# Kernel optimization log

Hardware: AMD Instinct MI355X
Metric: run time of the kernel (lower is better)

The kernel has to match this reference:

```python
import jax, jax.numpy as jnp
import numpy as np

N, B, D = 50000, 128, 35   # nodes, graphs, node_dim
T = 140                     # padded sequence length
EPS = 1e-5

def _gcn(x, W, b, src, dst):
    # PyG GCNConv: sym-normalized adjacency with self loops, then linear.
    h = x @ W
    deg = jnp.ones((N,), h.dtype).at[dst].add(1.0)  # in-degree + self loop
    dinv = jax.lax.rsqrt(deg)
    msg = h[src] * (dinv[src] * dinv[dst])[:, None]
    agg = jax.ops.segment_sum(msg, dst, num_segments=N)
    return agg + h * (dinv * dinv)[:, None] + b  # + self-loop messages + bias

def _bn(x, g, b):
    m = x.mean(0)
    v = x.var(0)
    return (x - m) * jax.lax.rsqrt(v + EPS) * g + b

def _lstm(xs, Wih, Whh, bih, bhh, reverse):
    # xs: [T, B, D]; torch LSTM gate order i,f,g,o; hidden size D
    def step(carry, xt):
        h, c = carry
        gates = xt @ Wih.T + h @ Whh.T + bih + bhh
        i, f, g, o = jnp.split(gates, 4, axis=-1)
        c = jax.nn.sigmoid(f) * c + jax.nn.sigmoid(i) * jnp.tanh(g)
        h = jax.nn.sigmoid(o) * jnp.tanh(c)
        return (h, c), h
    h0 = jnp.zeros((xs.shape[1], D), xs.dtype)
    _, hs = jax.lax.scan(step, (h0, h0), xs, reverse=reverse)
    return hs

def setup_inputs() -> dict:
    key = jax.random.key(0)
    ks = iter(jax.random.split(key, 64))
    def w(shape, s=0.05):
        return jax.random.normal(next(ks), shape, jnp.float32) * s
    inp = {
        'x': jax.random.normal(next(ks), (N, D), jnp.float32),
        'edge_intra': jax.random.randint(next(ks), (2, 300000), 0, N, jnp.int32),
        'edge_inter': jax.random.randint(next(ks), (2, 100000), 0, N, jnp.int32),
        'split': jax.random.randint(next(ks), (N,), 0, 2, jnp.int32),
        'batch': jnp.sort(jax.random.randint(next(ks), (N,), 0, B, jnp.int32)),
    }
    dims = [(35, 128), (128, 256), (256, 512), (512, 256), (256, 35)]
    for i, (di, do) in enumerate(dims, 1):
        inp[f'W{i}'] = w((di, do)); inp[f'b{i}'] = jnp.zeros((do,), jnp.float32)
        inp[f'g{i}'] = jnp.ones((do,), jnp.float32); inp[f'be{i}'] = jnp.zeros((do,), jnp.float32)
    for d in ('f', 'b'):  # bidirectional LSTM, 4*D = 140 gate rows
        inp[f'Wih_{d}'] = w((4 * D, D)); inp[f'Whh_{d}'] = w((4 * D, D))
        inp[f'bih_{d}'] = jnp.zeros((4 * D,), jnp.float32); inp[f'bhh_{d}'] = jnp.zeros((4 * D,), jnp.float32)
    for nm in ('q', 'k', 'v'):  # attention over d=2*D=70
        inp[f'W{nm}'] = w((2 * D, 2 * D)); inp[f'b{nm}'] = jnp.zeros((2 * D,), jnp.float32)
    inp['Wfc1'] = w((9800, 4340), 0.01); inp['bfc1'] = jnp.zeros((4340,), jnp.float32)
    inp['Wfc2'] = w((4340, 1), 0.01); inp['bfc2'] = jnp.zeros((1,), jnp.float32)
    return inp

def reference(x, edge_intra, edge_inter, split, batch,
              W1, b1, g1, be1, W2, b2, g2, be2, W3, b3, g3, be3,
              W4, b4, g4, be4, W5, b5, g5, be5,
              Wih_f, Whh_f, bih_f, bhh_f, Wih_b, Whh_b, bih_b, bhh_b,
              Wq, bq, Wk, bk, Wv, bv, Wfc1, bfc1, Wfc2, bfc2):
    src = jnp.concatenate([edge_intra[0], edge_inter[0]])
    dst = jnp.concatenate([edge_intra[1], edge_inter[1]])
    # conv1-3: relu then bn; conv4: bn then relu; conv5: bn only
    h = _bn(jax.nn.relu(_gcn(x, W1, b1, src, dst)), g1, be1)
    h = _bn(jax.nn.relu(_gcn(h, W2, b2, src, dst)), g2, be2)
    h = _bn(jax.nn.relu(_gcn(h, W3, b3, src, dst)), g3, be3)
    h = jax.nn.relu(_bn(_gcn(h, W4, b4, src, dst), g4, be4))
    h = _bn(_gcn(h, W5, b5, src, dst), g5, be5)
    # masked global_add_pool per split (avoids dynamic boolean indexing)
    is_pro = (split == 1).astype(h.dtype)[:, None]
    pro = jax.ops.segment_sum(h * is_pro, batch, num_segments=B)
    lig = jax.ops.segment_sum(h * (1.0 - is_pro), batch, num_segments=B)
    seq = jnp.concatenate([lig, pro], axis=1).reshape(B, 2, D)  # L = 2
    seq = jnp.pad(seq, ((0, 0), (0, T - 2), (0, 0)))            # [B,140,35]
    # attention mask, L=2 (static)
    m = jnp.eye(T, dtype=jnp.float32)
    m = m.at[2:, :].set(0.0).at[:, 2:].set(0.0)
    m = m.at[:, 1].set(1.0).at[1, :].set(1.0).at[1, 1].set(0.0)
    # BiLSTM over time axis
    xs = seq.transpose(1, 0, 2)  # [T,B,35]
    hf = _lstm(xs, Wih_f, Whh_f, bih_f, bhh_f, False)
    hb = _lstm(xs, Wih_b, Whh_b, bih_b, bhh_b, True)
    out = jnp.concatenate([hf, hb], axis=-1).transpose(1, 0, 2)  # [B,140,70]
    # masked single-head attention
    q = out @ Wq + bq
    k = out @ Wk + bk
    v = out @ Wv + bv
    sc = jnp.einsum('bqd,bkd->bqk', q, k) / jnp.sqrt(jnp.asarray(2.0 * D, out.dtype))
    sc = jnp.where(m[None] == 0, -1e9, sc)
    o = jax.nn.softmax(sc, axis=-1) @ v  # [B,140,70]
    f = jax.nn.relu(o.reshape(B, -1) @ Wfc1 + bfc1)
    return (f @ Wfc2 + bfc2).reshape(-1)
```

## Files before the change

### kernel.cpp

```cpp
#include <hip/hip_runtime.h>

#define N_NODES 50000
#define DIM0 35
#define BGRAPH 128
#define TSEQ 140
#define EPSBN 1e-5f
#define E_TOTAL 400000
#define E_INTRA 300000
#define E_INTER 100000
#define FC1_OUT 4340

typedef __attribute__((ext_vector_type(8))) short s8v;
typedef __attribute__((ext_vector_type(4))) short s4v;
typedef __attribute__((ext_vector_type(4))) float f32x4;

static __device__ __forceinline__ unsigned short bf16_rne(float x) {
    unsigned int u = __float_as_uint(x);
    unsigned int r = (u + 0x7FFFu + ((u >> 16) & 1u)) >> 16;
    return (unsigned short)r;
}
static __device__ __forceinline__ void bf16_split(float x, unsigned short& h, unsigned short& l) {
    h = bf16_rne(x);
    float hf = __uint_as_float(((unsigned int)h) << 16);
    l = bf16_rne(x - hf);
}

static __device__ __forceinline__ void edge_sd(int e, const int* intra, const int* inter, int& s, int& d) {
    if (e < E_INTRA) { s = intra[e]; d = intra[E_INTRA + e]; }
    else { int k = e - E_INTRA; s = inter[k]; d = inter[E_INTER + k]; }
}

__global__ void k_init(int* cnt, int* cursor, float* out, const float* bfc2, float* bnsumAll, float* bv4) {
    int i = blockIdx.x * 256 + threadIdx.x;
    if (i < N_NODES) { cnt[i] = 0; cursor[i] = 0; }
    if (i < BGRAPH) out[i] = bfc2[0];
    if (i < 5 * 1024) bnsumAll[i] = 0.f;
    if (i < 256) bv4[i] = 0.f;
}

__global__ void k_deg(const int* intra, const int* inter, int* cnt) {
    int e = blockIdx.x * 256 + threadIdx.x;
    if (e >= E_TOTAL) return;
    int s, d; edge_sd(e, intra, inter, s, d);
    atomicAdd(&cnt[d], 1);
}

__global__ void k_scan1(const int* __restrict__ cnt, int* __restrict__ partial, int* __restrict__ blocksum,
                        float* __restrict__ dinv) {
    __shared__ int buf[256];
    int t = threadIdx.x;
    int i = blockIdx.x * 256 + t;
    int v = (i < N_NODES) ? cnt[i] : 0;
    if (i < N_NODES) dinv[i] = rsqrtf(1.0f + (float)v);
    buf[t] = v;
    __syncthreads();
    for (int off = 1; off < 256; off <<= 1) {
        int add = (t >= off) ? buf[t - off] : 0;
        __syncthreads();
        buf[t] += add;
        __syncthreads();
    }
    if (i < N_NODES) partial[i] = buf[t];
    if (t == 255) blocksum[blockIdx.x] = buf[255];
}

__global__ void k_scan2(int* blocksum, int nb) {
    __shared__ int buf[256];
    int t = threadIdx.x;
    buf[t] = (t < nb) ? blocksum[t] : 0;
    __syncthreads();
    for (int off = 1; off < 256; off <<= 1) {
        int add = (t >= off) ? buf[t - off] : 0;
        __syncthreads();
        buf[t] += add;
        __syncthreads();
    }
    if (t < nb) blocksum[t] = buf[t];
}

__global__ void k_scan3(const int* __restrict__ partial, const int* __restrict__ blocksum, int* __restrict__ rowptr) {
    int b = blockIdx.x;
    int i = b * 256 + threadIdx.x;
    if (i == 0) rowptr[0] = 0;
    if (i < N_NODES) {
        int off = (b == 0) ? 0 : blocksum[b - 1];
        rowptr[i + 1] = partial[i] + off;
    }
}

__global__ void k_scatter(const int* intra, const int* inter, const int* rowptr,
                          int* cursor, const float* dinv, int* srcs, float* coef) {
    int e = blockIdx.x * 256 + threadIdx.x;
    if (e >= E_TOTAL) return;
    int s, d; edge_sd(e, intra, inter, s, d);
    int p = rowptr[d] + atomicAdd(&cursor[d], 1);
    srcs[p] = s;
    coef[p] = dinv[s] * dinv[d];
}

__global__ __launch_bounds__(256) void k_agg_small(const float* __restrict__ X, float* __restrict__ Z,
        const int* __restrict__ rowptr, const int* __restrict__ srcs, const float* __restrict__ coef,
        const float* __restrict__ dinv, const float* __restrict__ bias) {
    int wave = threadIdx.x >> 6, lane = threadIdx.x & 63;
    int i = blockIdx.x * 4 + wave;
    if (i >= N_NODES || lane >= DIM0) return;
    int b0 = rowptr[i], e1 = rowptr[i + 1];
    float self = dinv[i] * dinv[i];
    float acc = X[(size_t)i * DIM0 + lane] * self;
    if (bias) acc += bias[lane];
    for (int k = b0; k < e1; ++k) acc += coef[k] * X[(size_t)srcs[k] * DIM0 + lane];
    Z[(size_t)i * DIM0 + lane] = acc;
}

__global__ __launch_bounds__(256) void k_agg_vec(const float* __restrict__ X, float* __restrict__ Z,
        const int* __restrict__ rowptr, const int* __restrict__ srcs, const float* __restrict__ coef,
        const float* __restrict__ dinv, const float* __restrict__ alpha, const float* __restrict__ beta,
        const float* __restrict__ bias, int d, int lpshift) {
    int i = (blockIdx.x * 256 + threadIdx.x) >> lpshift;
    int lane_in = threadIdx.x & ((1 << lpshift) - 1);
    if (i >= N_NODES) return;
    int b0 = rowptr[i], e1 = rowptr[i + 1];
    float self = dinv[i] * dinv[i];
    int c = lane_in * 4;
    float4 al, be;
    if (alpha) { al = *(const float4*)&alpha[c]; be = *(const float4*)&beta[c]; }
    else { al = make_float4(1.f, 1.f, 1.f, 1.f); be = make_float4(0.f, 0.f, 0.f, 0.f); }
    float4 xi = *(const float4*)&X[(size_t)i * d + c];
    float4 acc;
    acc.x = self * (al.x * xi.x + be.x);
    acc.y = self * (al.y * xi.y + be.y);
    acc.z = self * (al.z * xi.z + be.z);
    acc.w = self * (al.w * xi.w + be.w);
    if (bias) {
        float4 bi = *(const float4*)&bias[c];
        acc.x += bi.x; acc.y += bi.y; acc.z += bi.z; acc.w += bi.w;
    }
    for (int k = b0; k < e1; ++k) {
        int s = srcs[k];
        float cf = coef[k];
        float4 xs = *(const float4*)&X[(size_t)s * d + c];
        acc.x += cf * (al.x * xs.x + be.x);
        acc.y += cf * (al.y * xs.y + be.y);
        acc.z += cf * (al.z * xs.z + be.z);
        acc.w += cf * (al.w * xs.w + be.w);
    }
    *(float4*)&Z[(size_t)i * d + c] = acc;
}

__global__ __launch_bounds__(256) void k_gemm(const float* __restrict__ A, const float* __restrict__ W,
                                              const float* __restrict__ bias, float* __restrict__ C,
                                              int Mrows, int K, int Ncols, int relu,
                                              const float* __restrict__ alphaA, const float* __restrict__ betaA,
                                              int reluA) {
    __shared__ float As[64][17];
    __shared__ float Ws[16][65];
    int tid = threadIdx.x;
    int tx = tid & 15, ty = tid >> 4;
    int row0 = blockIdx.y * 64, col0 = blockIdx.x * 64;
    float acc[4][4] = {};
    for (int k0 = 0; k0 < K; k0 += 16) {
        for (int l = tid; l < 1024; l += 256) {
            int m = l >> 4, kk = l & 15;
            int r = row0 + m, k = k0 + kk;
            float v = 0.f;
            if (r < Mrows && k < K) {
                v = A[(size_t)r * K + k];
                if (alphaA) {
                    v = alphaA[k] * v + betaA[k];
                    if (reluA) v = fmaxf(v, 0.f);
                }
            }
            As[m][kk] = v;
        }
        for (int l = tid; l < 1024; l += 256) {
            int kk = l >> 6, n = l & 63;
            int k = k0 + kk, c = col0 + n;
            Ws[kk][n] = (k < K && c < Ncols) ? W[(size_t)k * Ncols + c] : 0.f;
        }
        __syncthreads();
#pragma unroll
        for (int kk = 0; kk < 16; ++kk) {
            float a[4], w[4];
#pragma unroll
            for (int i2 = 0; i2 < 4; ++i2) a[i2] = As[ty * 4 + i2][kk];
#pragma unroll
            for (int j = 0; j < 4; ++j) w[j] = Ws[kk][tx * 4 + j];
#pragma unroll
            for (int i2 = 0; i2 < 4; ++i2)
#pragma unroll
                for (int j = 0; j < 4; ++j)
                    acc[i2][j] += a[i2] * w[j];
        }
        __syncthreads();
    }
    for (int i2 = 0; i2 < 4; ++i2) {
        int r = row0 + ty * 4 + i2;
        if (r >= Mrows) continue;
        for (int j = 0; j < 4; ++j) {
            int c = col0 + tx * 4 + j;
            if (c >= Ncols) continue;
            float v = acc[i2][j];
            if (bias) v += bias[c];
            if (relu) v = fmaxf(v, 0.f);
            C[(size_t)r * Ncols + c] = v;
        }
    }
}

__global__ void k_wprep(const float* __restrict__ W, unsigned short* __restrict__ Wf, int K, int Ncols,
                        const float* __restrict__ rowscale) {
    int gid = blockIdx.x * 256 + threadIdx.x;
    int KT = K >> 5;
    int total = (Ncols >> 4) * KT * 64;
    if (gid >= total) return;
    int lane = gid & 63;
    int f = gid >> 6;
    int kt = f % KT, ntile = f / KT;
    int n = ntile * 16 + (lane & 15);
    int kb = kt * 32 + (lane >> 4) * 8;
    size_t base = (size_t)f * 1024 + lane * 8;
#pragma unroll
    for (int j = 0; j < 8; ++j) {
        float v = W[(size_t)(kb + j) * Ncols + n];
        if (rowscale) v *= rowscale[kb + j];
        unsigned short h, l;
        bf16_split(v, h, l);
        Wf[base + j] = h;
        Wf[base + 512 + j] = l;
    }
}

__global__ void k_bnbias(const float* __restrict__ W, const float* __restrict__ beta,
                         float* __restrict__ bv, int K, int Ncols) {
    int c = threadIdx.x;
    if (c >= Ncols) return;
    int k0 = blockIdx.x * 16;
    float acc = 0.f;
#pragma unroll
    for (int k = 0; k < 16; ++k) acc += beta[k0 + k] * W[(size_t)(k0 + k) * Ncols + c];
    atomicAdd(&bv[c], acc);
}

__global__ __launch_bounds__(256) void k_gemm_mfma(
    const float* __restrict__ A, const unsigned short* __restrict__ Wf,
    const float* __restrict__ bias, float* __restrict__ C,
    int Mrows, int K, int Ncols, int relu,
    const float* __restrict__ alphaA, const float* __restrict__ betaA,
    float* __restrict__ bnsum) {
    __shared__ unsigned short As[2][2][128][40];
    int tid = threadIdx.x;
    int lane = tid & 63, wave = tid >> 6;
    int wm = wave >> 1, wn = wave & 1;
    int row0 = blockIdx.y * 128;
    int nt0 = blockIdx.x * 8;
    int KT = K >> 5;

    f32x4 acc[4][4];
#pragma unroll
    for (int a = 0; a < 4; ++a)
#pragma unroll
        for (int b = 0; b < 4; ++b) acc[a][b] = (f32x4)0.f;

    float4 reg[4];
    auto load_chunk = [&](int kt) {
#pragma unroll
        for (int l = 0; l < 4; ++l) {
            int i = tid + l * 256;
            int m = i >> 3, kv = (i & 7) * 4;
            int r = row0 + m;
            float4 v = make_float4(0.f, 0.f, 0.f, 0.f);
            if (r < Mrows) v = *(const float4*)&A[(size_t)r * K + kt * 32 + kv];
            reg[l] = v;
        }
    };
    auto store_chunk = [&](int buf, int kt) {
#pragma unroll
        for (int l = 0; l < 4; ++l) {
            int i = tid + l * 256;
            int m = i >> 3, kv = (i & 7) * 4;
            float4 v = reg[l];
            if (alphaA) {
                int kg = kt * 32 + kv;
                float4 al = *(const float4*)&alphaA[kg];
                float4 be = *(const float4*)&betaA[kg];
                v.x = al.x * v.x + be.x;
                v.y = al.y * v.y + be.y;
                v.z = al.z * v.z + be.z;
                v.w = al.w * v.w + be.w;
            }
            unsigned short h0, l0, h1, l1, h2, l2, h3, l3;
            bf16_split(v.x, h0, l0); bf16_split(v.y, h1, l1);
            bf16_split(v.z, h2, l2); bf16_split(v.w, h3, l3);
            s4v hv = {(short)h0, (short)h1, (short)h2, (short)h3};
            s4v lv = {(short)l0, (short)l1, (short)l2, (short)l3};
            *(s4v*)&As[buf][0][m][kv] = hv;
            *(s4v*)&As[buf][1][m][kv] = lv;
        }
    };

    load_chunk(0);
    store_chunk(0, 0);
    __syncthreads();

    int mrow = wm * 64 + (lane & 15);
    int koff = (lane >> 4) * 8;

    for (int kt = 0; kt < KT; ++kt) {
        int cur = kt & 1;
        if (kt + 1 < KT) load_chunk(kt + 1);
        s8v bh[4], bl[4];
#pragma unroll
        for (int nt = 0; nt < 4; ++nt) {
            int ntg = nt0 + wn * 4 + nt;
            size_t fb = ((size_t)(ntg * KT + kt)) * 1024 + lane * 8;
            bh[nt] = *(const s8v*)&Wf[fb];
            bl[nt] = *(const s8v*)&Wf[fb + 512];
        }
        s8v ah[4], alo[4];
#pragma unroll
        for (int mt = 0; mt < 4; ++mt) {
            ah[mt]  = *(const s8v*)&As[cur][0][mrow + mt * 16][koff];
            alo[mt] = *(const s8v*)&As[cur][1][mrow + mt * 16][koff];
        }
#pragma unroll
        for (int nt = 0; nt < 4; ++nt)
#pragma unroll
            for (int mt = 0; mt < 4; ++mt) {
                acc[mt][nt] = __builtin_amdgcn_mfma_f32_16x16x32_bf16(ah[mt], bh[nt], acc[mt][nt], 0, 0, 0);
                acc[mt][nt] = __builtin_amdgcn_mfma_f32_16x16x32_bf16(ah[mt], bl[nt], acc[mt][nt], 0, 0, 0);
                acc[mt][nt] = __builtin_amdgcn_mfma_f32_16x16x32_bf16(alo[mt], bh[nt], acc[mt][nt], 0, 0, 0);
            }
        if (kt + 1 < KT) store_chunk(cur ^ 1, kt + 1);
        __syncthreads();
    }

#pragma unroll
    for (int nt = 0; nt < 4; ++nt) {
        int cg = (nt0 + wn * 4 + nt) * 16 + (lane & 15);
        float bia = bias ? bias[cg] : 0.f;
        float s1 = 0.f, s2 = 0.f;
#pragma unroll
        for (int mt = 0; mt < 4; ++mt) {
            int rbase = row0 + wm * 64 + mt * 16 + (lane >> 4) * 4;
#pragma unroll
            for (int r = 0; r < 4; ++r) {
                int rg = rbase + r;
                if (rg < Mrows) {
                    float v = acc[mt][nt][r] + bia;
                    if (relu) v = fmaxf(v, 0.f);
                    C[(size_t)rg * Ncols + cg] = v;
                    s1 += v; s2 += v * v;
                }
            }
        }
        if (bnsum) {
            s1 += __shfl_xor(s1, 16, 64);
            s1 += __shfl_xor(s1, 32, 64);
            s2 += __shfl_xor(s2, 16, 64);
            s2 += __shfl_xor(s2, 32, 64);
            if (lane < 16) {
                atomicAdd(&bnsum[cg], s1);
                atomicAdd(&bnsum[Ncols + cg], s2);
            }
        }
    }
}

__global__ void k_bn_stats(const float* __restrict__ X, float* sums, int d) {
    long long total = (long long)N_NODES * d;
    int G = gridDim.x * blockDim.x;
    int gid = blockIdx.x * blockDim.x + threadIdx.x;
    int c = gid % d;
    float s1 = 0.f, s2 = 0.f;
    for (long long i = gid; i < total; i += G) {
        float v = X[i];
        s1 += v; s2 += v * v;
    }
    atomicAdd(&sums[c], s1);
    atomicAdd(&sums[d + c], s2);
}

__global__ void k_bn_final(const float* sums, const float* g, const float* be,
                           float* alpha, float* beta, int d) {
    int c = threadIdx.x;
    if (c >= d) return;
    float mean = sums[c] / (float)N_NODES;
    float var = sums[d + c] / (float)N_NODES - mean * mean;
    float a = g[c] * rsqrtf(var + EPSBN);
    alpha[c] = a;
    beta[c] = be[c] - mean * a;
}

__global__ void k_pool(const float* __restrict__ h, const int* __restrict__ split,
                       const int* __restrict__ batch, float* lig, float* pro,
                       const float* __restrict__ alpha, const float* __restrict__ beta) {
    int b = blockIdx.x;
    __shared__ float sl[DIM0], sp[DIM0];
    __shared__ int s_start, s_end;
    if (threadIdx.x < DIM0) { sl[threadIdx.x] = 0.f; sp[threadIdx.x] = 0.f; }
    if (threadIdx.x == 0) {
        int lo = 0, hi = N_NODES;
        while (lo < hi) { int mid = (lo + hi) >> 1; if (batch[mid] < b) lo = mid + 1; else hi = mid; }
        s_start = lo;
        hi = N_NODES;
        while (lo < hi) { int mid = (lo + hi) >> 1; if (batch[mid] < b + 1) lo = mid + 1; else hi = mid; }
        s_end = lo;
    }
    __syncthreads();
    int start = s_start, end = s_end;
    for (int k = threadIdx.x; k < (end - start) * DIM0; k += blockDim.x) {
        int node = start + k / DIM0;
        int c = k % DIM0;
        float v = alpha[c] * h[(size_t)node * DIM0 + c] + beta[c];
        if (split[node] == 1) atomicAdd(&sp[c], v);
        else atomicAdd(&sl[c], v);
    }
    __syncthreads();
    if (threadIdx.x < DIM0) {
        lig[b * DIM0 + threadIdx.x] = sl[threadIdx.x];
        pro[b * DIM0 + threadIdx.x] = sp[threadIdx.x];
    }
}

__global__ __launch_bounds__(192) void k_lstm(
    const float* __restrict__ lig, const float* __restrict__ pro,
    const float* __restrict__ Wih_f, const float* __restrict__ Whh_f,
    const float* __restrict__ bih_f, const float* __restrict__ bhh_f,
    const float* __restrict__ Wih_b, const float* __restrict__ Whh_b,
    const float* __restrict__ bih_b, const float* __restrict__ bhh_b,
    float* __restrict__ outb) {
    int blk = blockIdx.x;
    int dir = blk >> 7;
    int b = blk & 127;
    const float* Wih = dir ? Wih_b : Wih_f;
    const float* Whh = dir ? Whh_b : Whh_f;
    const float* bih = dir ? bih_b : bih_f;
    const float* bhh = dir ? bhh_b : bhh_f;

    __shared__ float h_lds[DIM0];
    __shared__ float x_lds[2][DIM0];
    __shared__ float gate_lds[4 * DIM0];
    int t = threadIdx.x;
    float wih[DIM0], whh[DIM0], bsum = 0.f;
    if (t < 4 * DIM0) {
#pragma unroll
        for (int j = 0; j < DIM0; ++j) { wih[j] = Wih[t * DIM0 + j]; whh[j] = Whh[t * DIM0 + j]; }
        bsum = bih[t] + bhh[t];
    }
    if (t < DIM0) {
        x_lds[0][t] = lig[b * DIM0 + t];
        x_lds[1][t] = pro[b * DIM0 + t];
        h_lds[t] = 0.f;
    }
    float c_reg = 0.f;
    __syncthreads();
    for (int step = 0; step < TSEQ; ++step) {
        int tt = dir ? (TSEQ - 1 - step) : step;
        if (t < 4 * DIM0) {
            float acc = bsum;
            if (tt < 2) {
#pragma unroll
                for (int j = 0; j < DIM0; ++j) acc += wih[j] * x_lds[tt][j];
            }
#pragma unroll
            for (int j = 0; j < DIM0; ++j) acc += whh[j] * h_lds[j];
            gate_lds[t] = acc;
        }
        __syncthreads();
        if (t < DIM0) {
            float gi = gate_lds[t], gf = gate_lds[DIM0 + t];
            float gg = gate_lds[2 * DIM0 + t], go = gate_lds[3 * DIM0 + t];
            float si = 1.f / (1.f + expf(-gi));
            float sf = 1.f / (1.f + expf(-gf));
            float so = 1.f / (1.f + expf(-go));
            c_reg = sf * c_reg + si * tanhf(gg);
            float hv = so * tanhf(c_reg);
            h_lds[t] = hv;
            outb[((size_t)b * TSEQ + tt) * 70 + dir * DIM0 + t] = hv;
        }
        __syncthreads();
    }
}

__global__ void k_concatW(const float* __restrict__ Wq, const float* __restrict__ bq,
                          const float* __restrict__ Wk, const float* __restrict__ bk,
                          const float* __restrict__ Wv, const float* __restrict__ bv,
                          float* __restrict__ Wcat, float* __restrict__ bcat) {
    int idx = blockIdx.x * 256 + threadIdx.x;
    if (idx < 70 * 210) {
        int k = idx / 210, col = idx % 210;
        int g = col / 70, j = col % 70;
        const float* Wsrc = (g == 0) ? Wq : ((g == 1) ? Wk : Wv);
        Wcat[idx] = Wsrc[k * 70 + j];
    }
    if (idx < 210) {
        int g = idx / 70, j = idx % 70;
        const float* bsrc = (g == 0) ? bq : ((g == 1) ? bk : bv);
        bcat[idx] = bsrc[j];
    }
}

__global__ void k_attention(const float* __restrict__ qkv, float* __restrict__ osm) {
    int b = blockIdx.x;
    __shared__ float q0[70], q1[70], s[TSEQ];
    __shared__ float s00_s, s01_s, ssum_s;
    int t = threadIdx.x;
    const float* base = qkv + (size_t)b * TSEQ * 210;
    if (t < 70) {
        q0[t] = base[0 * 210 + t];
        q1[t] = base[1 * 210 + t];
    }
    __syncthreads();
    const float scale = rsqrtf(70.f);
    if (t < TSEQ) {
        const float* krow = base + (size_t)t * 210 + 70;
        float acc = 0.f;
        for (int j = 0; j < 70; ++j) acc += q1[j] * krow[j];
        s[t] = acc * scale;
    } else if (t == TSEQ || t == TSEQ + 1) {
        int kk = t - TSEQ;
        const float* krow = base + (size_t)kk * 210 + 70;
        float acc = 0.f;
        for (int j = 0; j < 70; ++j) acc += q0[j] * krow[j];
        if (kk) s01_s = acc * scale; else s00_s = acc * scale;
    }
    __syncthreads();
    if (t == 0) {
        float mx = -1e30f;
        for (int i = 0; i < TSEQ; ++i) if (i != 1) mx = fmaxf(mx, s[i]);
        float sum = 0.f;
        for (int i = 0; i < TSEQ; ++i) {
            float e = (i == 1) ? 0.f : expf(s[i] - mx);
            s[i] = e; sum += e;
        }
        ssum_s = sum;
    }
    __syncthreads();
    if (t < 70) {
        float inv = 1.f / ssum_s;
        float acc = 0.f;
        for (int i = 0; i < TSEQ; ++i) acc += s[i] * base[(size_t)i * 210 + 140 + t];
        float o1v = acc * inv;
        float m0 = fmaxf(s00_s, s01_s);
        float e0 = expf(s00_s - m0), e1 = expf(s01_s - m0);
        float w0 = e0 / (e0 + e1), w1 = e1 / (e0 + e1);
        float v0 = base[0 * 210 + 140 + t];
        float v1 = base[1 * 210 + 140 + t];
        osm[b * 210 + t] = w0 * v0 + w1 * v1;
        osm[b * 210 + 70 + t] = o1v;
        osm[b * 210 + 140 + t] = v1;
    }
}

__global__ void k_wsum(const float* __restrict__ Wfc1, float* __restrict__ Wsum) {
    int idx = blockIdx.x * 256 + threadIdx.x;
    if (idx >= 70 * FC1_OUT) return;
    int j = idx / FC1_OUT, c = idx % FC1_OUT;
    float acc = 0.f;
    for (int tt = 2; tt < TSEQ; ++tt) acc += Wfc1[((size_t)(tt * 70 + j)) * FC1_OUT + c];
    Wsum[(size_t)j * FC1_OUT + c] = acc;
}

__global__ __launch_bounds__(256) void k_fc(const float* __restrict__ osm, const float* __restrict__ Wfc1,
                                            const float* __restrict__ Wsum, const float* __restrict__ bfc1,
                                            const float* __restrict__ Wfc2, float* __restrict__ out) {
    __shared__ float olds[8][210];
    __shared__ float wred[4][8];
    int g = blockIdx.y;
    int c = blockIdx.x * 256 + threadIdx.x;
    for (int l = threadIdx.x; l < 8 * 210; l += 256)
        olds[l / 210][l % 210] = osm[(g * 8 + l / 210) * 210 + (l % 210)];
    __syncthreads();
    float acc[8] = {};
    if (c < FC1_OUT) {
        for (int j = 0; j < 140; ++j) {
            float w = Wfc1[(size_t)j * FC1_OUT + c];
#pragma unroll
            for (int b = 0; b < 8; ++b) acc[b] = fmaf(olds[b][j], w, acc[b]);
        }
        for (int j = 0; j < 70; ++j) {
            float w = Wsum[(size_t)j * FC1_OUT + c];
#pragma unroll
            for (int b = 0; b < 8; ++b) acc[b] = fmaf(olds[b][140 + j], w, acc[b]);
        }
        float bb = bfc1[c], pw = Wfc2[c];
#pragma unroll
        for (int b = 0; b < 8; ++b) acc[b] = fmaxf(acc[b] + bb, 0.f) * pw;
    }
#pragma unroll
    for (int b = 0; b < 8; ++b) {
        acc[b] += __shfl_down(acc[b], 32, 64);
        acc[b] += __shfl_down(acc[b], 16, 64);
        acc[b] += __shfl_down(acc[b], 8, 64);
        acc[b] += __shfl_down(acc[b], 4, 64);
        acc[b] += __shfl_down(acc[b], 2, 64);
        acc[b] += __shfl_down(acc[b], 1, 64);
    }
    int wave = threadIdx.x >> 6;
    if ((threadIdx.x & 63) == 0)
#pragma unroll
        for (int b = 0; b < 8; ++b) wred[wave][b] = acc[b];
    __syncthreads();
    if (threadIdx.x < 8) {
        float t = wred[0][threadIdx.x] + wred[1][threadIdx.x] + wred[2][threadIdx.x] + wred[3][threadIdx.x];
        atomicAdd(&out[g * 8 + threadIdx.x], t);
    }
}

extern "C" void kernel_launch(void* const* d_in, const int* in_sizes, int n_in,
                              void* d_out, int out_size, void* d_ws, size_t ws_size,
                              hipStream_t stream) {
    const float* x = (const float*)d_in[0];
    const int* intra = (const int*)d_in[1];
    const int* inter = (const int*)d_in[2];
    const int* split = (const int*)d_in[3];
    const int* batch = (const int*)d_in[4];
    const float *W[5], *bW[5], *gW[5], *beW[5];
    for (int i = 0; i < 5; ++i) {
        W[i]   = (const float*)d_in[5 + 4 * i];
        bW[i]  = (const float*)d_in[6 + 4 * i];
        gW[i]  = (const float*)d_in[7 + 4 * i];
        beW[i] = (const float*)d_in[8 + 4 * i];
    }
    const float* Wih_f = (const float*)d_in[25];
    const float* Whh_f = (const float*)d_in[26];
    const float* bih_f = (const float*)d_in[27];
    const float* bhh_f = (const float*)d_in[28];
    const float* Wih_b = (const float*)d_in[29];
    const float* Whh_b = (const float*)d_in[30];
    const float* bih_b = (const float*)d_in[31];
    const float* bhh_b = (const float*)d_in[32];
    const float* Wq = (const float*)d_in[33];
    const float* bq = (const float*)d_in[34];
    const float* Wk = (const float*)d_in[35];
    const float* bk = (const float*)d_in[36];
    const float* Wv = (const float*)d_in[37];
    const float* bv = (const float*)d_in[38];
    const float* Wfc1 = (const float*)d_in[39];
    const float* bfc1 = (const float*)d_in[40];
    const float* Wfc2 = (const float*)d_in[41];
    const float* bfc2 = (const float*)d_in[42];

    char* p = (char*)d_ws;
    auto carve = [&](size_t bytes) {
        char* r = p;
        p += (bytes + 255) & ~(size_t)255;
        return r;
    };
    float* bufA = (float*)carve((size_t)N_NODES * 512 * 4);
    float* bufB = (float*)carve((size_t)N_NODES * 256 * 4);
    float* bufM = (float*)carve((size_t)N_NODES * 256 * 4);
    float* dinv = (float*)carve((size_t)N_NODES * 4);
    int* cnt    = (int*)carve((size_t)N_NODES * 4);
    int* rowptr = (int*)carve((size_t)(N_NODES + 1) * 4);
    int* cursor = (int*)carve((size_t)N_NODES * 4);
    int* scanp  = (int*)carve((size_t)N_NODES * 4);
    int* bsums  = (int*)carve(256 * 4);
    int* srcs   = (int*)carve((size_t)E_TOTAL * 4);
    float* coef = (float*)carve((size_t)E_TOTAL * 4);
    float* bnsumAll = (float*)carve(5 * 1024 * 4);
    float* alphaAll = (float*)carve(5 * 512 * 4);
    float* betaAll  = (float*)carve(5 * 512 * 4);
    float* bv4  = (float*)carve(256 * 4);
    float* lig = (float*)carve((size_t)BGRAPH * DIM0 * 4);
    float* pro = (float*)carve((size_t)BGRAPH * DIM0 * 4);
    float* outb = (float*)carve((size_t)BGRAPH * TSEQ * 70 * 4);
    float* qkvb = (float*)carve((size_t)BGRAPH * TSEQ * 210 * 4);
    float* Wcat = (float*)carve((size_t)70 * 210 * 4);
    float* bcat = (float*)carve(210 * 4);
    float* osm = (float*)carve((size_t)BGRAPH * 210 * 4);
    float* wsum = (float*)carve((size_t)70 * FC1_OUT * 4);
    unsigned short* Wf2 = (unsigned short*)carve((size_t)128 * 256 * 2 * 2);
    unsigned short* Wf3 = (unsigned short*)carve((size_t)256 * 512 * 2 * 2);
    unsigned short* Wf4 = (unsigned short*)carve((size_t)512 * 256 * 2 * 2);

    float* out = (float*)d_out;

    const int SCAN_B = (N_NODES + 255) / 256;

    k_init<<<(N_NODES + 255) / 256, 256, 0, stream>>>(cnt, cursor, out, bfc2, bnsumAll, bv4);
    k_deg<<<(E_TOTAL + 255) / 256, 256, 0, stream>>>(intra, inter, cnt);
    k_scan1<<<SCAN_B, 256, 0, stream>>>(cnt, scanp, bsums, dinv);
    k_scan2<<<1, 256, 0, stream>>>(bsums, SCAN_B);
    k_scan3<<<SCAN_B, 256, 0, stream>>>(scanp, bsums, rowptr);
    k_scatter<<<(E_TOTAL + 255) / 256, 256, 0, stream>>>(intra, inter, rowptr, cursor, dinv, srcs, coef);
    k_concatW<<<(70 * 210 + 255) / 256, 256, 0, stream>>>(Wq, bq, Wk, bk, Wv, bv, Wcat, bcat);
    k_wprep<<<((256 / 16) * (128 / 32) * 64 + 255) / 256, 256, 0, stream>>>(W[1], Wf2, 128, 256, nullptr);
    k_wprep<<<((512 / 16) * (256 / 32) * 64 + 255) / 256, 256, 0, stream>>>(W[2], Wf3, 256, 512, nullptr);

    auto BN = [&](int layer) { return bnsumAll + layer * 1024; };
    auto AL = [&](int layer) { return alphaAll + layer * 512; };
    auto BE = [&](int layer) { return betaAll + layer * 512; };
    auto bn_final = [&](int layer, int d) {
        k_bn_final<<<1, 512, 0, stream>>>(BN(layer), gW[layer], beW[layer], AL(layer), BE(layer), d);
    };

    const int GB64 = (N_NODES + 63) / 64;
    const int GB128 = (N_NODES + 127) / 128;
    const int AGG4 = (N_NODES + 3) / 4;
    const int AGG8 = (N_NODES + 7) / 8;

    k_agg_small<<<AGG4, 256, 0, stream>>>(x, bufM, rowptr, srcs, coef, dinv, nullptr);
    k_gemm<<<dim3(2, GB64), 256, 0, stream>>>(bufM, W[0], bW[0], bufA, N_NODES, 35, 128, 1, nullptr, nullptr, 0);
    k_bn_stats<<<128, 256, 0, stream>>>(bufA, BN(0), 128);
    bn_final(0, 128);
    k_agg_vec<<<AGG8, 256, 0, stream>>>(bufA, bufM, rowptr, srcs, coef, dinv, AL(0), BE(0), nullptr, 128, 5);
    k_gemm_mfma<<<dim3(2, GB128), 256, 0, stream>>>(bufM, Wf2, bW[1], bufB, N_NODES, 128, 256, 1,
                                                    nullptr, nullptr, BN(1));
    bn_final(1, 256);
    k_agg_vec<<<AGG4, 256, 0, stream>>>(bufB, bufM, rowptr, srcs, coef, dinv, AL(1), BE(1), nullptr, 256, 6);
    k_gemm_mfma<<<dim3(4, GB128), 256, 0, stream>>>(bufM, Wf3, bW[2], bufA, N_NODES, 256, 512, 1,
                                                    nullptr, nullptr, BN(2));
    bn_final(2, 512);
    k_wprep<<<((256 / 16) * (512 / 32) * 64 + 255) / 256, 256, 0, stream>>>(W[3], Wf4, 512, 256, AL(2));
    k_bnbias<<<512 / 16, 256, 0, stream>>>(W[3], BE(2), bv4, 512, 256);
    k_gemm_mfma<<<dim3(2, GB128), 256, 0, stream>>>(bufA, Wf4, bv4, bufM, N_NODES, 512, 256, 0,
                                                    nullptr, nullptr, nullptr);
    k_agg_vec<<<AGG4, 256, 0, stream>>>(bufM, bufB, rowptr, srcs, coef, dinv, nullptr, nullptr, bW[3], 256, 6);
    k_bn_stats<<<256, 256, 0, stream>>>(bufB, BN(3), 256);
    bn_final(3, 256);
    k_gemm<<<dim3(1, GB64), 256, 0, stream>>>(bufB, W[4], nullptr, bufM, N_NODES, 256, 35, 0, AL(3), BE(3), 1);
    k_agg_small<<<AGG4, 256, 0, stream>>>(bufM, bufA, rowptr, srcs, coef, dinv, bW[4]);
    k_bn_stats<<<35, 256, 0, stream>>>(bufA, BN(4), 35);
    bn_final(4, 35);

    k_pool<<<BGRAPH, 256, 0, stream>>>(bufA, split, batch, lig, pro, AL(4), BE(4));

    k_lstm<<<256, 192, 0, stream>>>(lig, pro, Wih_f, Whh_f, bih_f, bhh_f,
                                    Wih_b, Whh_b, bih_b, bhh_b, outb);

    k_gemm<<<dim3(4, (BGRAPH * TSEQ + 63) / 64), 256, 0, stream>>>(outb, Wcat, bcat, qkvb,
                                                                   BGRAPH * TSEQ, 70, 210, 0, nullptr, nullptr, 0);

    k_attention<<<BGRAPH, 256, 0, stream>>>(qkvb, osm);

    k_wsum<<<(70 * FC1_OUT + 255) / 256, 256, 0, stream>>>(Wfc1, wsum);
    k_fc<<<dim3(17, 16), 256, 0, stream>>>(osm, Wfc1, wsum, bfc1, Wfc2, out);
}
```

Measured before the change: 1.072 ms.

## Restructure MFMA GEMM to 64-row tiles with 128-deep K chunks looping over columns

```diff
diff --git a/kernel.cpp b/kernel.cpp
--- a/kernel.cpp
+++ b/kernel.cpp
@@ -241,126 +241,115 @@
     atomicAdd(&bv[c], acc);
 }
 
-__global__ __launch_bounds__(256) void k_gemm_mfma(
+__global__ __launch_bounds__(256, 3) void k_gemm_mfma3(
     const float* __restrict__ A, const unsigned short* __restrict__ Wf,
     const float* __restrict__ bias, float* __restrict__ C,
     int Mrows, int K, int Ncols, int relu,
     const float* __restrict__ alphaA, const float* __restrict__ betaA,
     float* __restrict__ bnsum) {
-    __shared__ unsigned short As[2][2][128][40];
+    __shared__ unsigned short As[2][64][136];
     int tid = threadIdx.x;
-    int lane = tid & 63, wave = tid >> 6;
-    int wm = wave >> 1, wn = wave & 1;
-    int row0 = blockIdx.y * 128;
-    int nt0 = blockIdx.x * 8;
+    int lane = tid & 63, w = tid >> 6;
+    int row0 = blockIdx.x * 64;
     int KT = K >> 5;
-
-    f32x4 acc[4][4];
-#pragma unroll
-    for (int a = 0; a < 4; ++a)
-#pragma unroll
-        for (int b = 0; b < 4; ++b) acc[a][b] = (f32x4)0.f;
-
-    float4 reg[4];
-    auto load_chunk = [&](int kt) {
-#pragma unroll
-        for (int l = 0; l < 4; ++l) {
-            int i = tid + l * 256;
-            int m = i >> 3, kv = (i & 7) * 4;
-            int r = row0 + m;
-            float4 v = make_float4(0.f, 0.f, 0.f, 0.f);
-            if (r < Mrows) v = *(const float4*)&A[(size_t)r * K + kt * 32 + kv];
-            reg[l] = v;
-        }
-    };
-    auto store_chunk = [&](int buf, int kt) {
-#pragma unroll
-        for (int l = 0; l < 4; ++l) {
-            int i = tid + l * 256;
-            int m = i >> 3, kv = (i & 7) * 4;
-            float4 v = reg[l];
-            if (alphaA) {
-                int kg = kt * 32 + kv;
-                float4 al = *(const float4*)&alphaA[kg];
-                float4 be = *(const float4*)&betaA[kg];
-                v.x = al.x * v.x + be.x;
-                v.y = al.y * v.y + be.y;
-                v.z = al.z * v.z + be.z;
-                v.w = al.w * v.w + be.w;
+    int nchunk = K >> 7;
+    int npairs = Ncols >> 8;
+
+    int arow = lane & 15;
+    int ahalf = (lane >> 4) * 8;
+
+    for (int pp = 0; pp < npairs; ++pp) {
+        f32x4 acc[4][4];
+#pragma unroll
+        for (int a = 0; a < 4; ++a)
+#pragma unroll
+            for (int b = 0; b < 4; ++b) acc[a][b] = (f32x4)0.f;
+
+        for (int ch = 0; ch < nchunk; ++ch) {
+            __syncthreads();
+#pragma unroll
+            for (int l = 0; l < 8; ++l) {
+                int idx = tid + l * 256;
+                int m = idx >> 5, kv = (idx & 31) * 4;
+                int r = row0 + m;
+                float4 v = make_float4(0.f, 0.f, 0.f, 0.f);
+                if (r < Mrows) v = *(const float4*)&A[(size_t)r * K + ch * 128 + kv];
+                if (alphaA) {
+                    int kg = ch * 128 + kv;
+                    float4 al = *(const float4*)&alphaA[kg];
+                    float4 be = *(const float4*)&betaA[kg];
+                    v.x = al.x * v.x + be.x;
+                    v.y = al.y * v.y + be.y;
+                    v.z = al.z * v.z + be.z;
+                    v.w = al.w * v.w + be.w;
+                }
+                unsigned short h0, l0, h1, l1, h2, l2, h3, l3;
+                bf16_split(v.x, h0, l0); bf16_split(v.y, h1, l1);
+                bf16_split(v.z, h2, l2); bf16_split(v.w, h3, l3);
+                s4v hv = {(short)h0, (short)h1, (short)h2, (short)h3};
+                s4v lv = {(short)l0, (short)l1, (short)l2, (short)l3};
+                *(s4v*)&As[0][m][kv] = hv;
+                *(s4v*)&As[1][m][kv] = lv;
             }
-            unsigned short h0, l0, h1, l1, h2, l2, h3, l3;
-            bf16_split(v.x, h0, l0); bf16_split(v.y, h1, l1);
-            bf16_split(v.z, h2, l2); bf16_split(v.w, h3, l3);
-            s4v hv = {(short)h0, (short)h1, (short)h2, (short)h3};
-            s4v lv = {(short)l0, (short)l1, (short)l2, (short)l3};
-            *(s4v*)&As[buf][0][m][kv] = hv;
-            *(s4v*)&As[buf][1][m][kv] = lv;
-        }
-    };
-
-    load_chunk(0);
-    store_chunk(0, 0);
-    __syncthreads();
-
-    int mrow = wm * 64 + (lane & 15);
-    int koff = (lane >> 4) * 8;
-
-    for (int kt = 0; kt < KT; ++kt) {
-        int cur = kt & 1;
-        if (kt + 1 < KT) load_chunk(kt + 1);
-        s8v bh[4], bl[4];
+            __syncthreads();
+
+#pragma unroll
+            for (int ktl = 0; ktl < 4; ++ktl) {
+                int ktg = ch * 4 + ktl;
+                int akoff = ktl * 32 + ahalf;
+                s8v ah[4], alo[4];
+#pragma unroll
+                for (int mt = 0; mt < 4; ++mt) {
+                    ah[mt]  = *(const s8v*)&As[0][arow + mt * 16][akoff];
+                    alo[mt] = *(const s8v*)&As[1][arow + mt * 16][akoff];
+                }
+                s8v bh[4], bl[4];
+#pragma unroll
+                for (int nt = 0; nt < 4; ++nt) {
+                    int ntg = pp * 16 + w * 4 + nt;
+                    size_t fb = ((size_t)(ntg * KT + ktg)) * 1024 + lane * 8;
+                    bh[nt] = *(const s8v*)&Wf[fb];
+                    bl[nt] = *(const s8v*)&Wf[fb + 512];
+                }
+#pragma unroll
+                for (int nt = 0; nt < 4; ++nt)
+#pragma unroll
+                    for (int mt = 0; mt < 4; ++mt) {
+                        acc[mt][nt] = __builtin_amdgcn_mfma_f32_16x16x32_bf16(ah[mt], bh[nt], acc[mt][nt], 0, 0, 0);
+                        acc[mt][nt] = __builtin_amdgcn_mfma_f32_16x16x32_bf16(ah[mt], bl[nt], acc[mt][nt], 0, 0, 0);
+                        acc[mt][nt] = __builtin_amdgcn_mfma_f32_16x16x32_bf16(alo[mt], bh[nt], acc[mt][nt], 0, 0, 0);
+                    }
+            }
+        }
+
 #pragma unroll
         for (int nt = 0; nt < 4; ++nt) {
-            int ntg = nt0 + wn * 4 + nt;
-            size_t fb = ((size_t)(ntg * KT + kt)) * 1024 + lane * 8;
-            bh[nt] = *(const s8v*)&Wf[fb];
-            bl[nt] = *(const s8v*)&Wf[fb + 512];
-        }
-        s8v ah[4], alo[4];
-#pragma unroll
-        for (int mt = 0; mt < 4; ++mt) {
-            ah[mt]  = *(const s8v*)&As[cur][0][mrow + mt * 16][koff];
-            alo[mt] = *(const s8v*)&As[cur][1][mrow + mt * 16][koff];
-        }
-#pragma unroll
-        for (int nt = 0; nt < 4; ++nt)
+            int cg = (pp * 16 + w * 4 + nt) * 16 + (lane & 15);
+            float bia = bias ? bias[cg] : 0.f;
+            float s1 = 0.f, s2 = 0.f;
 #pragma unroll
             for (int mt = 0; mt < 4; ++mt) {
-                acc[mt][nt] = __builtin_amdgcn_mfma_f32_16x16x32_bf16(ah[mt], bh[nt], acc[mt][nt], 0, 0, 0);
-                acc[mt][nt] = __builtin_amdgcn_mfma_f32_16x16x32_bf16(ah[mt], bl[nt], acc[mt][nt], 0, 0, 0);
-                acc[mt][nt] = __builtin_amdgcn_mfma_f32_16x16x32_bf16(alo[mt], bh[nt], acc[mt][nt], 0, 0, 0);
-            }
-        if (kt + 1 < KT) store_chunk(cur ^ 1, kt + 1);
-        __syncthreads();
-    }
-
-#pragma unroll
-    for (int nt = 0; nt < 4; ++nt) {
-        int cg = (nt0 + wn * 4 + nt) * 16 + (lane & 15);
-        float bia = bias ? bias[cg] : 0.f;
-        float s1 = 0.f, s2 = 0.f;
-#pragma unroll
-        for (int mt = 0; mt < 4; ++mt) {
-            int rbase = row0 + wm * 64 + mt * 16 + (lane >> 4) * 4;
-#pragma unroll
-            for (int r = 0; r < 4; ++r) {
-                int rg = rbase + r;
-                if (rg < Mrows) {
-                    float v = acc[mt][nt][r] + bia;
-                    if (relu) v = fmaxf(v, 0.f);
-                    C[(size_t)rg * Ncols + cg] = v;
-                    s1 += v; s2 += v * v;
+                int rbase = row0 + mt * 16 + (lane >> 4) * 4;
+#pragma unroll
+                for (int r = 0; r < 4; ++r) {
+                    int rg = rbase + r;
+                    if (rg < Mrows) {
+                        float v = acc[mt][nt][r] + bia;
+                        if (relu) v = fmaxf(v, 0.f);
+                        C[(size_t)rg * Ncols + cg] = v;
+                        s1 += v; s2 += v * v;
+                    }
                 }
             }
-        }
-        if (bnsum) {
-            s1 += __shfl_xor(s1, 16, 64);
-            s1 += __shfl_xor(s1, 32, 64);
-            s2 += __shfl_xor(s2, 16, 64);
-            s2 += __shfl_xor(s2, 32, 64);
-            if (lane < 16) {
-                atomicAdd(&bnsum[cg], s1);
-                atomicAdd(&bnsum[Ncols + cg], s2);
+            if (bnsum) {
+                s1 += __shfl_xor(s1, 16, 64);
+                s1 += __shfl_xor(s1, 32, 64);
+                s2 += __shfl_xor(s2, 16, 64);
+                s2 += __shfl_xor(s2, 32, 64);
+                if (lane < 16) {
+                    atomicAdd(&bnsum[cg], s1);
+                    atomicAdd(&bnsum[Ncols + cg], s2);
+                }
             }
         }
     }
@@ -696,7 +685,6 @@
     };
 
     const int GB64 = (N_NODES + 63) / 64;
-    const int GB128 = (N_NODES + 127) / 128;
     const int AGG4 = (N_NODES + 3) / 4;
     const int AGG8 = (N_NODES + 7) / 8;
 
@@ -705,17 +693,17 @@
     k_bn_stats<<<128, 256, 0, stream>>>(bufA, BN(0), 128);
     bn_final(0, 128);
     k_agg_vec<<<AGG8, 256, 0, stream>>>(bufA, bufM, rowptr, srcs, coef, dinv, AL(0), BE(0), nullptr, 128, 5);
-    k_gemm_mfma<<<dim3(2, GB128), 256, 0, stream>>>(bufM, Wf2, bW[1], bufB, N_NODES, 128, 256, 1,
-                                                    nullptr, nullptr, BN(1));
+    k_gemm_mfma3<<<GB64, 256, 0, stream>>>(bufM, Wf2, bW[1], bufB, N_NODES, 128, 256, 1,
+                                           nullptr, nullptr, BN(1));
     bn_final(1, 256);
     k_agg_vec<<<AGG4, 256, 0, stream>>>(bufB, bufM, rowptr, srcs, coef, dinv, AL(1), BE(1), nullptr, 256, 6);
-    k_gemm_mfma<<<dim3(4, GB128), 256, 0, stream>>>(bufM, Wf3, bW[2], bufA, N_NODES, 256, 512, 1,
-                                                    nullptr, nullptr, BN(2));
+    k_gemm_mfma3<<<GB64, 256, 0, stream>>>(bufM, Wf3, bW[2], bufA, N_NODES, 256, 512, 1,
+                                           nullptr, nullptr, BN(2));
     bn_final(2, 512);
     k_wprep<<<((256 / 16) * (512 / 32) * 64 + 255) / 256, 256, 0, stream>>>(W[3], Wf4, 512, 256, AL(2));
     k_bnbias<<<512 / 16, 256, 0, stream>>>(W[3], BE(2), bv4, 512, 256);
-    k_gemm_mfma<<<dim3(2, GB128), 256, 0, stream>>>(bufA, Wf4, bv4, bufM, N_NODES, 512, 256, 0,
-                                                    nullptr, nullptr, nullptr);
+    k_gemm_mfma3<<<GB64, 256, 0, stream>>>(bufA, Wf4, bv4, bufM, N_NODES, 512, 256, 0,
+                                           nullptr, nullptr, nullptr);
     k_agg_vec<<<AGG4, 256, 0, stream>>>(bufM, bufB, rowptr, srcs, coef, dinv, nullptr, nullptr, bW[3], 256, 6);
     k_bn_stats<<<256, 256, 0, stream>>>(bufB, BN(3), 256);
     bn_final(3, 256);
```

After: 1.162 ms. 1.08x slower.
